# Optimization experiments

Hardware: AMD Instinct MI355X
Metric: run time of the kernel (lower is better)

Reference implementation:

```python
import jax, jax.numpy as jnp
from jax import lax
import numpy as np

DIM = 384
HEADS = 8
SR = 2
B, D0, D1, D2 = 4, 16, 16, 16
N = 1 + D0 * D1 * D2


def setup_inputs() -> dict:
    key = jax.random.key(0)
    ks = jax.random.split(key, 8)
    s = 0.02
    return {
        "x": jax.random.normal(ks[0], (B, N, DIM), dtype=jnp.float32),
        "q_w": jax.random.normal(ks[1], (DIM, DIM), dtype=jnp.float32) * s,
        "kv_w": jax.random.normal(ks[2], (2 * DIM, DIM), dtype=jnp.float32) * s,
        "proj_w": jax.random.normal(ks[3], (DIM, DIM), dtype=jnp.float32) * s,
        "proj_b": jnp.zeros((DIM,), dtype=jnp.float32),
        "sr_w": jax.random.normal(ks[4], (DIM, 1, SR, SR, SR), dtype=jnp.float32) * s,  # depthwise (groups=dim)
        "sr_b": jnp.zeros((DIM,), dtype=jnp.float32),
        "ln_g": jnp.ones((DIM,), dtype=jnp.float32),
        "ln_b": jnp.zeros((DIM,), dtype=jnp.float32),
        "d0": D0, "d1": D1, "d2": D2,
    }


def reference(x, q_w, kv_w, proj_w, proj_b, sr_w, sr_b, ln_g, ln_b, d0, d1, d2):
    B_, N_, C = x.shape
    hd = C // HEADS
    scale = hd ** -0.5

    # q projection -> [B, H, N, hd]
    q = (x @ q_w.T).reshape(B_, N_, HEADS, hd).transpose(0, 2, 1, 3)

    # spatial reduction of patch tokens (keep CLS token)
    x_ = x[:, 1:].transpose(0, 2, 1).reshape(B_, C, d0, d1, d2)
    x_ = lax.conv_general_dilated(
        x_, sr_w, window_strides=(SR, SR, SR), padding="VALID",
        dimension_numbers=("NCDHW", "OIDHW", "NCDHW"), feature_group_count=C,
    ) + sr_b[None, :, None, None, None]
    x_ = x_.reshape(B_, C, -1).transpose(0, 2, 1)           # [B, M-1, C]
    x_ = jnp.concatenate([x[:, 0:1], x_], axis=1)            # [B, M, C]

    # LayerNorm (eps=1e-5)
    mu = jnp.mean(x_, axis=-1, keepdims=True)
    var = jnp.var(x_, axis=-1, keepdims=True)
    x_ = (x_ - mu) / jnp.sqrt(var + 1e-5) * ln_g + ln_b

    M = x_.shape[1]
    kv = (x_ @ kv_w.T).reshape(B_, M, 2, HEADS, hd).transpose(2, 0, 3, 1, 4)
    k, v = kv[0], kv[1]                                      # [B, H, M, hd]

    attn = jax.nn.softmax(jnp.einsum("bhnd,bhmd->bhnm", q, k) * scale, axis=-1)
    out = jnp.einsum("bhnm,bhmd->bhnd", attn, v)
    out = out.transpose(0, 2, 1, 3).reshape(B_, N_, C)
    return out @ proj_w.T + proj_b
```

## Files before the change

### kernel.cpp

```cpp
#include <hip/hip_runtime.h>

typedef unsigned short u16;
typedef unsigned int u32;
typedef __bf16 bf16x8 __attribute__((ext_vector_type(8)));
typedef float f32x4 __attribute__((ext_vector_type(4)));

#define NTOK 4097
#define MTOK 513
#define MPAD 544
#define KPAD 640
#define NPAD_Q 4224
#define ROWS_X 16512

__device__ __forceinline__ u16 f2bf(float f) {
  u32 u = __builtin_bit_cast(u32, f);
  u = u + 0x7FFFu + ((u >> 16) & 1u);
  return (u16)(u >> 16);
}
__device__ __forceinline__ u16 f2bf_fast(float f) {
  u32 u = __builtin_bit_cast(u32, f);
  return (u16)((u + 0x8000u) >> 16);
}

__device__ __forceinline__ void gld16(const u16* g, u16* l) {
  __builtin_amdgcn_global_load_lds((const __attribute__((address_space(1))) u32*)g,
                                   (__attribute__((address_space(3))) u32*)l, 16, 0, 0);
}

#define NX   6292992
#define NQW  147456
#define NKVW 294912
#define NPW  147456
__global__ void cast_all(const float* __restrict__ x, const float* __restrict__ qw,
                         const float* __restrict__ kvw, const float* __restrict__ pw,
                         u16* __restrict__ xb, u16* __restrict__ qwb,
                         u16* __restrict__ kvwb, u16* __restrict__ pwb) {
  int i = blockIdx.x * blockDim.x + threadIdx.x;
  int stride = gridDim.x * blockDim.x;
  for (; i < NX + NQW + NKVW + NPW; i += stride) {
    const float* src;
    u16* dst;
    int off;
    if (i < NX) { src = x; dst = xb; off = i; }
    else if (i < NX + NQW) { src = qw; dst = qwb; off = i - NX; }
    else if (i < NX + NQW + NKVW) { src = kvw; dst = kvwb; off = i - (NX + NQW); }
    else { src = pw; dst = pwb; off = i - (NX + NQW + NKVW); }
    dst[off] = f2bf(src[off]);
  }
}

__global__ void sr_ln_kernel(const float* __restrict__ x, const float* __restrict__ srw,
                             const float* __restrict__ srb, const float* __restrict__ lng,
                             const float* __restrict__ lnb, u16* __restrict__ xln) {
  int c = threadIdx.x;
  int bm = blockIdx.x;
  int b = bm / MTOK, m = bm - b * MTOK;
  float v;
  if (m == 0) {
    v = x[(b * NTOK) * 384 + c];
  } else {
    int mo = m - 1;
    int oz = mo >> 6, oy = (mo >> 3) & 7, ox = mo & 7;
    float acc = srb[c];
#pragma unroll
    for (int dz = 0; dz < 2; dz++)
#pragma unroll
      for (int dy = 0; dy < 2; dy++)
#pragma unroll
        for (int dx = 0; dx < 2; dx++) {
          int tok = 1 + ((2 * oz + dz) * 256 + (2 * oy + dy) * 16 + (2 * ox + dx));
          acc += x[(b * NTOK + tok) * 384 + c] * srw[c * 8 + dz * 4 + dy * 2 + dx];
        }
    v = acc;
  }
  float s1 = v, s2 = v * v;
#pragma unroll
  for (int msk = 32; msk >= 1; msk >>= 1) {
    s1 += __shfl_xor(s1, msk);
    s2 += __shfl_xor(s2, msk);
  }
  __shared__ float r1[6], r2[6];
  int w = threadIdx.x >> 6, lane = threadIdx.x & 63;
  if (lane == 0) { r1[w] = s1; r2[w] = s2; }
  __syncthreads();
  float S1 = 0.f, S2 = 0.f;
#pragma unroll
  for (int i = 0; i < 6; i++) { S1 += r1[i]; S2 += r2[i]; }
  float mu = S1 * (1.0f / 384.0f);
  float var = S2 * (1.0f / 384.0f) - mu * mu;
  float y = (v - mu) * rsqrtf(var + 1e-5f) * lng[c] + lnb[c];
  xln[(b * MPAD + m) * 384 + c] = f2bf(y);
}

__global__ __launch_bounds__(256) void gemm_bt(const u16* __restrict__ A, const u16* __restrict__ W,
                                               int mode, u16* __restrict__ o1, u16* __restrict__ o2,
                                               float* __restrict__ of, const float* __restrict__ bias) {
  __shared__ __align__(16) u16 aLds[2][128 * 64];
  __shared__ __align__(16) u16 bLds[2][128 * 64];
  int tid = threadIdx.x, w = tid >> 6, lane = tid & 63, q4 = lane >> 4, c16 = lane & 15;
  int wr = w >> 1, wc = w & 1;
  int c0 = blockIdx.y * 128;
  size_t rbase = (size_t)blockIdx.x * 128;
  int x7 = c16 & 7;

  auto stageAB = [&](int kc, int buf) {
#pragma unroll
    for (int i = 0; i < 4; i++) {
      int s = (w * 4 + i) * 64 + lane;
      int row = s >> 3, chp = s & 7;
      int ch = chp ^ (row & 7);
      gld16(A + (rbase + row) * 384 + kc * 64 + ch * 8, &aLds[buf][(w * 4 + i) * 512]);
    }
#pragma unroll
    for (int i = 0; i < 4; i++) {
      int s = (w * 4 + i) * 64 + lane;
      int row = s >> 3, chp = s & 7;
      int ch = chp ^ (row & 7);
      gld16(W + (size_t)(c0 + row) * 384 + kc * 64 + ch * 8, &bLds[buf][(w * 4 + i) * 512]);
    }
  };
  stageAB(0, 0);
  __syncthreads();

  f32x4 acc[4][4];
#pragma unroll
  for (int mt = 0; mt < 4; mt++)
#pragma unroll
    for (int nt = 0; nt < 4; nt++) acc[mt][nt] = (f32x4){0, 0, 0, 0};

  for (int c = 0; c < 6; c++) {
    int cb = c & 1, nb = cb ^ 1;
    if (c < 5) stageAB(c + 1, nb);
#pragma unroll
    for (int ks = 0; ks < 2; ks++) {
      bf16x8 af[4], bf[4];
#pragma unroll
      for (int mt = 0; mt < 4; mt++)
        af[mt] = *(const bf16x8*)(&aLds[cb][(wr * 64 + mt * 16 + c16) * 64 + ((ks * 4 + q4) ^ x7) * 8]);
#pragma unroll
      for (int nt = 0; nt < 4; nt++)
        bf[nt] = *(const bf16x8*)(&bLds[cb][(wc * 64 + nt * 16 + c16) * 64 + ((ks * 4 + q4) ^ x7) * 8]);
#pragma unroll
      for (int mt = 0; mt < 4; mt++)
#pragma unroll
        for (int nt = 0; nt < 4; nt++)
          acc[mt][nt] = __builtin_amdgcn_mfma_f32_16x16x32_bf16(af[mt], bf[nt], acc[mt][nt], 0, 0, 0);
    }
    __syncthreads();
  }

#pragma unroll
  for (int mt = 0; mt < 4; mt++)
#pragma unroll
    for (int nt = 0; nt < 4; nt++) {
      int col = c0 + wc * 64 + nt * 16 + c16;
#pragma unroll
      for (int r = 0; r < 4; r++) {
        int R = (int)rbase + wr * 64 + mt * 16 + q4 * 4 + r;
        float val = acc[mt][nt][r];
        if (mode == 0) {
          int b = R / NTOK;
          if (b >= 4) continue;
          int n = R - b * NTOK;
          int h = col / 48, d = col - h * 48;
          o1[((size_t)(b * 8 + h) * NPAD_Q + n) * 64 + d] = f2bf(val * 0.14433756729740643f);
        } else if (mode == 1) {
          int b = R / MPAD;
          int m = R - b * MPAD;
          if (col < 384) {
            int h = col / 48, d = col - h * 48;
            o1[((size_t)(b * 8 + h) * KPAD + m) * 64 + d] = f2bf(val);
          } else {
            int c2 = col - 384;
            int h = c2 / 48, d = c2 - h * 48;
            o2[((size_t)(b * 8 + h) * 48 + d) * KPAD + m] = f2bf(val);
          }
        } else {
          if (R < 4 * NTOK) of[(size_t)R * 384 + col] = val + bias[col];
        }
      }
    }
}

__global__ __launch_bounds__(256, 4) void attn_kernel(const u16* __restrict__ qb,
                                                      const u16* __restrict__ kb,
                                                      const u16* __restrict__ vt,
                                                      u16* __restrict__ outb) {
  __shared__ __align__(16) u16 klds[2][64][64];
  __shared__ __align__(16) u16 vlds[2][48][64];
  __shared__ __align__(16) u16 plds[4][16][76];
  int tid = threadIdx.x, w = tid >> 6, lane = tid & 63, q4 = lane >> 4, c16 = lane & 15;
  int bh = blockIdx.x;
  int n0 = blockIdx.y * 128 + w * 32;
  int r7 = c16 & 7;

  const uint4* qp = (const uint4*)(qb + ((size_t)bh * NPAD_Q + n0 + c16) * 64);
  bf16x8 aq[2][2];
#pragma unroll
  for (int rg = 0; rg < 2; rg++) {
    aq[rg][0] = __builtin_bit_cast(bf16x8, qp[rg * 128 + q4]);
    aq[rg][1] = __builtin_bit_cast(bf16x8, qp[rg * 128 + 4 + q4]);
  }

  const u16* kbase = kb + (size_t)bh * KPAD * 64;
  const u16* vbase = vt + (size_t)bh * 48 * KPAD;

  auto stage = [&](int cn, int buf) {
#pragma unroll
    for (int i = 0; i < 2; i++) {
      int s = (w * 2 + i) * 64 + lane;
      int row = s >> 3, chp = s & 7;
      int ch = chp ^ (row & 7);
      gld16(kbase + (size_t)(cn * 64 + row) * 64 + ch * 8, &klds[buf][(w * 2 + i) * 8][0]);
    }
#pragma unroll
    for (int i = 0; i < 2; i++) {
      int blk = w * 2 + i;
      if (blk < 6) {
        int s = blk * 64 + lane;
        int row = s >> 3, chp = s & 7;
        int ch = chp ^ (row & 7);
        gld16(vbase + (size_t)row * KPAD + cn * 64 + ch * 8, &vlds[buf][blk * 8][0]);
      }
    }
  };

  stage(0, 0);
  __syncthreads();

  f32x4 o[2][3];
  float lsum[2][4];
#pragma unroll
  for (int rg = 0; rg < 2; rg++) {
#pragma unroll
    for (int nt = 0; nt < 3; nt++) o[rg][nt] = (f32x4){0, 0, 0, 0};
#pragma unroll
    for (int r = 0; r < 4; r++) lsum[rg][r] = 0.f;
  }

  for (int c = 0; c < 8; c++) {
    int cb = c & 1, nb = cb ^ 1;
    stage(c + 1, nb);

    f32x4 s[2][4];
#pragma unroll
    for (int rg = 0; rg < 2; rg++)
#pragma unroll
      for (int t = 0; t < 4; t++) s[rg][t] = (f32x4){0, 0, 0, 0};
#pragma unroll
    for (int t = 0; t < 4; t++) {
      const u16* krow = &klds[cb][t * 16 + c16][0];
      bf16x8 k0 = *(const bf16x8*)(krow + (q4 ^ r7) * 8);
      bf16x8 k1 = *(const bf16x8*)(krow + ((q4 ^ r7) ^ 4) * 8);
#pragma unroll
      for (int rg = 0; rg < 2; rg++) {
        s[rg][t] = __builtin_amdgcn_mfma_f32_16x16x32_bf16(aq[rg][0], k0, s[rg][t], 0, 0, 0);
        s[rg][t] = __builtin_amdgcn_mfma_f32_16x16x32_bf16(aq[rg][1], k1, s[rg][t], 0, 0, 0);
      }
    }
#pragma unroll
    for (int rg = 0; rg < 2; rg++)
#pragma unroll
      for (int t = 0; t < 4; t++)
#pragma unroll
        for (int r = 0; r < 4; r++) {
          float e = __expf(s[rg][t][r]);
          s[rg][t][r] = e;
          lsum[rg][r] += e;
        }
    bf16x8 afrag[2][2];
#pragma unroll
    for (int rg = 0; rg < 2; rg++) {
#pragma unroll
      for (int t = 0; t < 4; t++)
#pragma unroll
        for (int r = 0; r < 4; r++) plds[w][q4 * 4 + r][t * 16 + c16] = f2bf_fast(s[rg][t][r]);
#pragma unroll
      for (int kl = 0; kl < 2; kl++)
        afrag[rg][kl] = *(const bf16x8*)(&plds[w][c16][kl * 32 + q4 * 8]);
    }
#pragma unroll
    for (int kl = 0; kl < 2; kl++)
#pragma unroll
      for (int nt = 0; nt < 3; nt++) {
        const u16* vrow = &vlds[cb][nt * 16 + c16][0];
        bf16x8 bv = *(const bf16x8*)(vrow + ((kl * 4 + q4) ^ r7) * 8);
#pragma unroll
        for (int rg = 0; rg < 2; rg++)
          o[rg][nt] = __builtin_amdgcn_mfma_f32_16x16x32_bf16(afrag[rg][kl], bv, o[rg][nt], 0, 0, 0);
      }
    __syncthreads();
  }

  {
    f32x4 s4[2] = {{0, 0, 0, 0}, {0, 0, 0, 0}};
    const u16* krow = &klds[0][c16][0];
    bf16x8 k0 = *(const bf16x8*)(krow + (q4 ^ r7) * 8);
    bf16x8 k1 = *(const bf16x8*)(krow + ((q4 ^ r7) ^ 4) * 8);
#pragma unroll
    for (int rg = 0; rg < 2; rg++) {
      s4[rg] = __builtin_amdgcn_mfma_f32_16x16x32_bf16(aq[rg][0], k0, s4[rg], 0, 0, 0);
      s4[rg] = __builtin_amdgcn_mfma_f32_16x16x32_bf16(aq[rg][1], k1, s4[rg], 0, 0, 0);
    }
    bf16x8 afrag[2];
#pragma unroll
    for (int rg = 0; rg < 2; rg++) {
#pragma unroll
      for (int r = 0; r < 4; r++) {
        float e = (c16 == 0) ? __expf(s4[rg][r]) : 0.f;
        lsum[rg][r] += e;
        plds[w][q4 * 4 + r][c16] = f2bf_fast(e);
        plds[w][q4 * 4 + r][16 + c16] = 0;
      }
      afrag[rg] = *(const bf16x8*)(&plds[w][c16][q4 * 8]);
    }
#pragma unroll
    for (int nt = 0; nt < 3; nt++) {
      const u16* vrow = &vlds[0][nt * 16 + c16][0];
      bf16x8 bv = *(const bf16x8*)(vrow + (q4 ^ r7) * 8);
#pragma unroll
      for (int rg = 0; rg < 2; rg++)
        o[rg][nt] = __builtin_amdgcn_mfma_f32_16x16x32_bf16(afrag[rg], bv, o[rg][nt], 0, 0, 0);
    }
  }

  int b = bh >> 3, h = bh & 7;
#pragma unroll
  for (int rg = 0; rg < 2; rg++) {
    float inv[4];
#pragma unroll
    for (int r = 0; r < 4; r++) {
      float l = lsum[rg][r];
      l += __shfl_xor(l, 1);
      l += __shfl_xor(l, 2);
      l += __shfl_xor(l, 4);
      l += __shfl_xor(l, 8);
      inv[r] = 1.0f / l;
    }
#pragma unroll
    for (int nt = 0; nt < 3; nt++)
#pragma unroll
      for (int r = 0; r < 4; r++) {
        int n = n0 + rg * 16 + q4 * 4 + r;
        if (n < NTOK) outb[((size_t)(b * NTOK + n)) * 384 + h * 48 + nt * 16 + c16] = f2bf(o[rg][nt][r] * inv[r]);
      }
  }
}

extern "C" void kernel_launch(void* const* d_in, const int* in_sizes, int n_in,
                              void* d_out, int out_size, void* d_ws, size_t ws_size,
                              hipStream_t stream) {
  const float* x = (const float*)d_in[0];
  const float* q_w = (const float*)d_in[1];
  const float* kv_w = (const float*)d_in[2];
  const float* proj_w = (const float*)d_in[3];
  const float* proj_b = (const float*)d_in[4];
  const float* sr_w = (const float*)d_in[5];
  const float* sr_b = (const float*)d_in[6];
  const float* ln_g = (const float*)d_in[7];
  const float* ln_b = (const float*)d_in[8];
  float* out = (float*)d_out;

  u16* ws = (u16*)d_ws;
  u16* x_b = ws;
  u16* qw_b = x_b + (size_t)ROWS_X * 384;
  u16* kvw_b = qw_b + 147456;
  u16* pw_b = kvw_b + 294912;
  u16* q_b = pw_b + 147456;
  u16* xln_b = q_b + (size_t)32 * NPAD_Q * 64;
  u16* k_b = xln_b + (size_t)4 * MPAD * 384;
  u16* vt_b = k_b + (size_t)32 * KPAD * 64;
  u16* attn_b = x_b;


  cast_all<<<8192, 256, 0, stream>>>(x, q_w, kv_w, proj_w, x_b, qw_b, kvw_b, pw_b);

  sr_ln_kernel<<<4 * MTOK, 384, 0, stream>>>(x, sr_w, sr_b, ln_g, ln_b, xln_b);

  gemm_bt<<<dim3(129, 3), 256, 0, stream>>>(x_b, qw_b, 0, q_b, nullptr, nullptr, nullptr);
  gemm_bt<<<dim3(17, 6), 256, 0, stream>>>(xln_b, kvw_b, 1, k_b, vt_b, nullptr, nullptr);
  attn_kernel<<<dim3(32, 33), 256, 0, stream>>>(q_b, k_b, vt_b, attn_b);
  gemm_bt<<<dim3(129, 3), 256, 0, stream>>>(attn_b, pw_b, 2, nullptr, nullptr, out, proj_b);
}
```

Measured before the change: 205.5 us.

## Merge cast and SR-LN kernels, vectorize cast, and fuse Q/KV GEMMs into one launch

The fp32-to-bf16 cast and the spatial-reduction+LayerNorm kernels become a single launch, with blocks split by index, and the cast now works on 8 elements per thread using float4 loads and uint4 stores. The Q and KV projection GEMMs are combined into one launch of 489 blocks that dispatch on block index to a shared GEMM core. This removes two kernel launches and their tail gaps, improves memory coalescing in the cast, and lets the small KV GEMM fill otherwise idle CUs during the Q GEMM. The cost is a mixed block-size grid (384 threads also used for the cast) and some extra branching.

```diff
diff --git a/kernel.cpp b/kernel.cpp
--- a/kernel.cpp
+++ b/kernel.cpp
@@ -31,76 +31,88 @@
 #define NQW  147456
 #define NKVW 294912
 #define NPW  147456
-__global__ void cast_all(const float* __restrict__ x, const float* __restrict__ qw,
-                         const float* __restrict__ kvw, const float* __restrict__ pw,
-                         u16* __restrict__ xb, u16* __restrict__ qwb,
-                         u16* __restrict__ kvwb, u16* __restrict__ pwb) {
-  int i = blockIdx.x * blockDim.x + threadIdx.x;
-  int stride = gridDim.x * blockDim.x;
-  for (; i < NX + NQW + NKVW + NPW; i += stride) {
-    const float* src;
-    u16* dst;
-    int off;
-    if (i < NX) { src = x; dst = xb; off = i; }
-    else if (i < NX + NQW) { src = qw; dst = qwb; off = i - NX; }
-    else if (i < NX + NQW + NKVW) { src = kvw; dst = kvwb; off = i - (NX + NQW); }
-    else { src = pw; dst = pwb; off = i - (NX + NQW + NKVW); }
-    dst[off] = f2bf(src[off]);
-  }
-}
-
-__global__ void sr_ln_kernel(const float* __restrict__ x, const float* __restrict__ srw,
-                             const float* __restrict__ srb, const float* __restrict__ lng,
-                             const float* __restrict__ lnb, u16* __restrict__ xln) {
-  int c = threadIdx.x;
-  int bm = blockIdx.x;
-  int b = bm / MTOK, m = bm - b * MTOK;
-  float v;
-  if (m == 0) {
-    v = x[(b * NTOK) * 384 + c];
+#define GX   (NX / 8)
+#define GQW  (NQW / 8)
+#define GKVW (NKVW / 8)
+#define GPW  (NPW / 8)
+#define GTOT (GX + GQW + GKVW + GPW)
+#define SRLN_BLOCKS (4 * MTOK)
+
+__global__ void pre_kernel(const float* __restrict__ x, const float* __restrict__ qw,
+                           const float* __restrict__ kvw, const float* __restrict__ pw,
+                           const float* __restrict__ srw, const float* __restrict__ srb,
+                           const float* __restrict__ lng, const float* __restrict__ lnb,
+                           u16* __restrict__ xb, u16* __restrict__ qwb,
+                           u16* __restrict__ kvwb, u16* __restrict__ pwb,
+                           u16* __restrict__ xln) {
+  if (blockIdx.x < SRLN_BLOCKS) {
+    int c = threadIdx.x;
+    int bm = blockIdx.x;
+    int b = bm / MTOK, m = bm - b * MTOK;
+    float v;
+    if (m == 0) {
+      v = x[(b * NTOK) * 384 + c];
+    } else {
+      int mo = m - 1;
+      int oz = mo >> 6, oy = (mo >> 3) & 7, ox = mo & 7;
+      float acc = srb[c];
+#pragma unroll
+      for (int dz = 0; dz < 2; dz++)
+#pragma unroll
+        for (int dy = 0; dy < 2; dy++)
+#pragma unroll
+          for (int dx = 0; dx < 2; dx++) {
+            int tok = 1 + ((2 * oz + dz) * 256 + (2 * oy + dy) * 16 + (2 * ox + dx));
+            acc += x[(b * NTOK + tok) * 384 + c] * srw[c * 8 + dz * 4 + dy * 2 + dx];
+          }
+      v = acc;
+    }
+    float s1 = v, s2 = v * v;
+#pragma unroll
+    for (int msk = 32; msk >= 1; msk >>= 1) {
+      s1 += __shfl_xor(s1, msk);
+      s2 += __shfl_xor(s2, msk);
+    }
+    __shared__ float r1[6], r2[6];
+    int w = threadIdx.x >> 6, lane = threadIdx.x & 63;
+    if (lane == 0) { r1[w] = s1; r2[w] = s2; }
+    __syncthreads();
+    float S1 = 0.f, S2 = 0.f;
+#pragma unroll
+    for (int i = 0; i < 6; i++) { S1 += r1[i]; S2 += r2[i]; }
+    float mu = S1 * (1.0f / 384.0f);
+    float var = S2 * (1.0f / 384.0f) - mu * mu;
+    float y = (v - mu) * rsqrtf(var + 1e-5f) * lng[c] + lnb[c];
+    xln[(b * MPAD + m) * 384 + c] = f2bf(y);
   } else {
-    int mo = m - 1;
-    int oz = mo >> 6, oy = (mo >> 3) & 7, ox = mo & 7;
-    float acc = srb[c];
-#pragma unroll
-    for (int dz = 0; dz < 2; dz++)
-#pragma unroll
-      for (int dy = 0; dy < 2; dy++)
-#pragma unroll
-        for (int dx = 0; dx < 2; dx++) {
-          int tok = 1 + ((2 * oz + dz) * 256 + (2 * oy + dy) * 16 + (2 * ox + dx));
-          acc += x[(b * NTOK + tok) * 384 + c] * srw[c * 8 + dz * 4 + dy * 2 + dx];
-        }
-    v = acc;
-  }
-  float s1 = v, s2 = v * v;
-#pragma unroll
-  for (int msk = 32; msk >= 1; msk >>= 1) {
-    s1 += __shfl_xor(s1, msk);
-    s2 += __shfl_xor(s2, msk);
-  }
-  __shared__ float r1[6], r2[6];
-  int w = threadIdx.x >> 6, lane = threadIdx.x & 63;
-  if (lane == 0) { r1[w] = s1; r2[w] = s2; }
-  __syncthreads();
-  float S1 = 0.f, S2 = 0.f;
-#pragma unroll
-  for (int i = 0; i < 6; i++) { S1 += r1[i]; S2 += r2[i]; }
-  float mu = S1 * (1.0f / 384.0f);
-  float var = S2 * (1.0f / 384.0f) - mu * mu;
-  float y = (v - mu) * rsqrtf(var + 1e-5f) * lng[c] + lnb[c];
-  xln[(b * MPAD + m) * 384 + c] = f2bf(y);
-}
-
-__global__ __launch_bounds__(256) void gemm_bt(const u16* __restrict__ A, const u16* __restrict__ W,
-                                               int mode, u16* __restrict__ o1, u16* __restrict__ o2,
-                                               float* __restrict__ of, const float* __restrict__ bias) {
-  __shared__ __align__(16) u16 aLds[2][128 * 64];
-  __shared__ __align__(16) u16 bLds[2][128 * 64];
+    int idx = (blockIdx.x - SRLN_BLOCKS) * blockDim.x + threadIdx.x;
+    int stride = (gridDim.x - SRLN_BLOCKS) * blockDim.x;
+    for (int g = idx; g < GTOT; g += stride) {
+      const float* s;
+      u16* d;
+      int off;
+      if (g < GX) { s = x; d = xb; off = g * 8; }
+      else if (g < GX + GQW) { s = qw; d = qwb; off = (g - GX) * 8; }
+      else if (g < GX + GQW + GKVW) { s = kvw; d = kvwb; off = (g - GX - GQW) * 8; }
+      else { s = pw; d = pwb; off = (g - GX - GQW - GKVW) * 8; }
+      float4 v0 = *(const float4*)(s + off);
+      float4 v1 = *(const float4*)(s + off + 4);
+      uint4 o;
+      u16* p = (u16*)&o;
+      p[0] = f2bf(v0.x); p[1] = f2bf(v0.y); p[2] = f2bf(v0.z); p[3] = f2bf(v0.w);
+      p[4] = f2bf(v1.x); p[5] = f2bf(v1.y); p[6] = f2bf(v1.z); p[7] = f2bf(v1.w);
+      *(uint4*)(d + off) = o;
+    }
+  }
+}
+
+__device__ __forceinline__ void gemm_core(u16* aLds, u16* bLds,
+                                          const u16* __restrict__ A, const u16* __restrict__ W,
+                                          int mode, size_t rbase, int c0,
+                                          u16* __restrict__ o1, u16* __restrict__ o2,
+                                          float* __restrict__ of, const float* __restrict__ bias) {
   int tid = threadIdx.x, w = tid >> 6, lane = tid & 63, q4 = lane >> 4, c16 = lane & 15;
   int wr = w >> 1, wc = w & 1;
-  int c0 = blockIdx.y * 128;
-  size_t rbase = (size_t)blockIdx.x * 128;
   int x7 = c16 & 7;
 
   auto stageAB = [&](int kc, int buf) {
@@ -109,14 +121,14 @@
       int s = (w * 4 + i) * 64 + lane;
       int row = s >> 3, chp = s & 7;
       int ch = chp ^ (row & 7);
-      gld16(A + (rbase + row) * 384 + kc * 64 + ch * 8, &aLds[buf][(w * 4 + i) * 512]);
+      gld16(A + (rbase + row) * 384 + kc * 64 + ch * 8, &aLds[buf * 8192 + (w * 4 + i) * 512]);
     }
 #pragma unroll
     for (int i = 0; i < 4; i++) {
       int s = (w * 4 + i) * 64 + lane;
       int row = s >> 3, chp = s & 7;
       int ch = chp ^ (row & 7);
-      gld16(W + (size_t)(c0 + row) * 384 + kc * 64 + ch * 8, &bLds[buf][(w * 4 + i) * 512]);
+      gld16(W + (size_t)(c0 + row) * 384 + kc * 64 + ch * 8, &bLds[buf * 8192 + (w * 4 + i) * 512]);
     }
   };
   stageAB(0, 0);
@@ -136,10 +148,10 @@
       bf16x8 af[4], bf[4];
 #pragma unroll
       for (int mt = 0; mt < 4; mt++)
-        af[mt] = *(const bf16x8*)(&aLds[cb][(wr * 64 + mt * 16 + c16) * 64 + ((ks * 4 + q4) ^ x7) * 8]);
+        af[mt] = *(const bf16x8*)(&aLds[cb * 8192 + (wr * 64 + mt * 16 + c16) * 64 + ((ks * 4 + q4) ^ x7) * 8]);
 #pragma unroll
       for (int nt = 0; nt < 4; nt++)
-        bf[nt] = *(const bf16x8*)(&bLds[cb][(wc * 64 + nt * 16 + c16) * 64 + ((ks * 4 + q4) ^ x7) * 8]);
+        bf[nt] = *(const bf16x8*)(&bLds[cb * 8192 + (wc * 64 + nt * 16 + c16) * 64 + ((ks * 4 + q4) ^ x7) * 8]);
 #pragma unroll
       for (int mt = 0; mt < 4; mt++)
 #pragma unroll
@@ -182,6 +194,31 @@
     }
 }
 
+__global__ __launch_bounds__(256) void gemm_qkv(const u16* __restrict__ xb, const u16* __restrict__ qwb,
+                                                const u16* __restrict__ xlnb, const u16* __restrict__ kvwb,
+                                                u16* __restrict__ qb, u16* __restrict__ kb2,
+                                                u16* __restrict__ vtb) {
+  __shared__ __align__(16) u16 aLds[2 * 128 * 64];
+  __shared__ __align__(16) u16 bLds[2 * 128 * 64];
+  int bx = blockIdx.x;
+  if (bx < 387) {
+    gemm_core(aLds, bLds, xb, qwb, 0, (size_t)(bx % 129) * 128, (bx / 129) * 128,
+              qb, nullptr, nullptr, nullptr);
+  } else {
+    int i = bx - 387;
+    gemm_core(aLds, bLds, xlnb, kvwb, 1, (size_t)(i % 17) * 128, (i / 17) * 128,
+              kb2, vtb, nullptr, nullptr);
+  }
+}
+
+__global__ __launch_bounds__(256) void gemm_out(const u16* __restrict__ A, const u16* __restrict__ W,
+                                                float* __restrict__ of, const float* __restrict__ bias) {
+  __shared__ __align__(16) u16 aLds[2 * 128 * 64];
+  __shared__ __align__(16) u16 bLds[2 * 128 * 64];
+  gemm_core(aLds, bLds, A, W, 2, (size_t)blockIdx.x * 128, blockIdx.y * 128,
+            nullptr, nullptr, of, bias);
+}
+
 __global__ __launch_bounds__(256, 4) void attn_kernel(const u16* __restrict__ qb,
                                                       const u16* __restrict__ kb,
                                                       const u16* __restrict__ vt,
@@ -373,12 +410,9 @@
   u16* attn_b = x_b;
 
 
-  cast_all<<<8192, 256, 0, stream>>>(x, q_w, kv_w, proj_w, x_b, qw_b, kvw_b, pw_b);
-
-  sr_ln_kernel<<<4 * MTOK, 384, 0, stream>>>(x, sr_w, sr_b, ln_g, ln_b, xln_b);
-
-  gemm_bt<<<dim3(129, 3), 256, 0, stream>>>(x_b, qw_b, 0, q_b, nullptr, nullptr, nullptr);
-  gemm_bt<<<dim3(17, 6), 256, 0, stream>>>(xln_b, kvw_b, 1, k_b, vt_b, nullptr, nullptr);
+  pre_kernel<<<SRLN_BLOCKS + 2240, 384, 0, stream>>>(x, q_w, kv_w, proj_w, sr_w, sr_b,
+                                                     ln_g, ln_b, x_b, qw_b, kvw_b, pw_b, xln_b);
+  gemm_qkv<<<489, 256, 0, stream>>>(x_b, qw_b, xln_b, kvw_b, q_b, k_b, vt_b);
   attn_kernel<<<dim3(32, 33), 256, 0, stream>>>(q_b, k_b, vt_b, attn_b);
-  gemm_bt<<<dim3(129, 3), 256, 0, stream>>>(attn_b, pw_b, 2, nullptr, nullptr, out, proj_b);
-}
+  gemm_out<<<dim3(129, 3), 256, 0, stream>>>(attn_b, pw_b, out, proj_b);
+}
```

Result: faster. 176.2 us (-14.3%).
